# Kernel optimization log

Measured on AMD Instinct MI355X. Metric: run time of the kernel, lower is better.

The kernel has to match this reference:

```python
import jax, jax.numpy as jnp
import numpy as np

N_NODES = 100000
N_EDGES = 1600000
D = 128          # gnn_input_size == gnn_hidden_size
N_LAYERS = 7
N_GRAPHS = 64
N_CLASSES = 10
SNN_IN, SNN_H = 512, 1024
SNN_BETA = 0.85


def setup_inputs() -> dict:
    key = jax.random.key(0)
    ks = jax.random.split(key, 16)
    s = 0.05  # keep activations tame through 7 relu layers
    return {
        "snn_x": jax.random.normal(ks[0], (N_GRAPHS, SNN_IN), jnp.float32),
        "x": jax.random.normal(ks[1], (N_NODES, D), jnp.float32),
        "edge_index": jax.random.randint(ks[2], (2, N_EDGES), 0, N_NODES, jnp.int64),
        "batch": jnp.sort(jax.random.randint(ks[3], (N_NODES,), 0, N_GRAPHS, jnp.int64)),
        "snn_w1": jax.random.normal(ks[4], (SNN_IN, SNN_H), jnp.float32) * s,
        "snn_b1": jax.random.normal(ks[5], (SNN_H,), jnp.float32) * s,
        "snn_w2": jax.random.normal(ks[6], (SNN_H, N_CLASSES), jnp.float32) * s,
        "snn_b2": jax.random.normal(ks[7], (N_CLASSES,), jnp.float32) * s,
        "conv_wrel": jax.random.normal(ks[8], (N_LAYERS, D, D), jnp.float32) * s,
        "conv_wroot": jax.random.normal(ks[9], (N_LAYERS, D, D), jnp.float32) * s,
        "conv_brel": jax.random.normal(ks[10], (N_LAYERS, D), jnp.float32) * s,
        "lin_w": jax.random.normal(ks[11], (D, N_CLASSES), jnp.float32) * s,
        "lin_b": jax.random.normal(ks[12], (N_CLASSES,), jnp.float32) * s,
        "fuse_w": jax.random.normal(ks[13], (2 * N_CLASSES, N_CLASSES), jnp.float32) * s,
        "fuse_b": jax.random.normal(ks[14], (N_CLASSES,), jnp.float32) * s,
    }


def reference(snn_x, x, edge_index, batch,
              snn_w1, snn_b1, snn_w2, snn_b2,
              conv_wrel, conv_wroot, conv_brel,
              lin_w, lin_b, fuse_w, fuse_b):
    n = x.shape[0]
    src, dst = edge_index[0], edge_index[1]
    h = x
    for i in range(conv_wrel.shape[0]):
        agg = jax.ops.segment_sum(h[src], dst, num_segments=n)  # gather + scatter-add
        h = jax.nn.relu(agg @ conv_wrel[i] + conv_brel[i] + h @ conv_wroot[i])
    # global_mean_pool over batch segments
    sums = jax.ops.segment_sum(h, batch, num_segments=N_GRAPHS)
    cnts = jax.ops.segment_sum(jnp.ones((n,), h.dtype), batch, num_segments=N_GRAPHS)
    pooled = sums / jnp.maximum(cnts, 1.0)[:, None]
    gnn_logits = pooled @ lin_w + lin_b
    # SNN branch
    snn_h = jax.nn.relu(snn_x @ snn_w1 + snn_b1)
    snn_logits = SNN_BETA * (snn_h @ snn_w2 + snn_b2)
    # fusion
    fused = jnp.concatenate([snn_logits, gnn_logits], axis=-1)
    return fused @ fuse_w + fuse_b
```

## Files before the change

### kernel.cpp

```cpp
#include <hip/hip_runtime.h>
#include <hip/hip_bf16.h>

#define N_NODES 100000
#define N_EDGES 1600000
#define DIM     128
#define N_LAYERS 7
#define N_GRAPHS 64
#define SNN_IN  512
#define SNN_HID 1024
#define NCLS    10
#define M_PAD   100096
#define MBLK    782
#define NBK     782
#define SORT_CHUNK 4096
#define SORT_NCH   391
#define XPAIRS  (N_NODES * 64)
#define HPAIRS  (M_PAD * 64)
#define WELEMS  (N_LAYERS * DIM * 256)
#define AGG_BLOCKS 2048
#define AGG_WAVES  (AGG_BLOCKS * 4)
#define NQUAD   (N_NODES / 4)
#define POOL2_NB 1564
#define SNN_BLKS 256
#define SS_PAD  2000384

#define AS1 __attribute__((address_space(1)))
#define AS3 __attribute__((address_space(3)))

typedef __attribute__((ext_vector_type(8))) short short8;
typedef __attribute__((ext_vector_type(4))) float f32x4;

__device__ __forceinline__ unsigned int f2bf(float f) {
    unsigned int u = __float_as_uint(f);
    return (u + 0x7fffu + ((u >> 16) & 1u)) >> 16;
}
__device__ __forceinline__ float bf2f(unsigned short b) {
    return __uint_as_float(((unsigned int)b) << 16);
}
__device__ __forceinline__ void acc_pair(unsigned int u, float& lo, float& hi) {
    lo += __uint_as_float(u << 16);
    hi += __uint_as_float(u & 0xffff0000u);
}

__global__ void k_convert(const float* __restrict__ x, const float* __restrict__ wrel,
                          const float* __restrict__ wroot, unsigned int* __restrict__ h,
                          unsigned short* __restrict__ Wt,
                          float* __restrict__ pooled, int* __restrict__ counts) {
    int i = blockIdx.x * blockDim.x + threadIdx.x;
    if (i < N_GRAPHS * 128) pooled[i] = 0.f;
    if (i >= N_GRAPHS * 128 && i < N_GRAPHS * 129) counts[i - N_GRAPHS * 128] = 0;
    if (i < XPAIRS) {
        float2 v = ((const float2*)x)[i];
        h[i] = f2bf(v.x) | (f2bf(v.y) << 16);
    } else if (i < HPAIRS) {
        h[i] = 0u;
    } else {
        int idx = i - HPAIRS;
        if (idx < WELEMS) {
            int l = idx >> 15, rem = idx & 32767, n = rem >> 8, k = rem & 255;
            float v = (k < 128) ? wrel[l * 16384 + k * 128 + n]
                                : wroot[l * 16384 + (k - 128) * 128 + n];
            Wt[idx] = (unsigned short)f2bf(v);
        }
    }
}

__global__ __launch_bounds__(256) void k_histA(const int* __restrict__ dst,
                                               int* __restrict__ chunk_hist) {
    __shared__ int hist[NBK];
    int b = blockIdx.x, t = threadIdx.x;
    int e0 = b * SORT_CHUNK;
    int e1 = e0 + SORT_CHUNK; if (e1 > N_EDGES) e1 = N_EDGES;
    for (int i = t; i < NBK; i += 256) hist[i] = 0;
    __syncthreads();
    for (int e = e0 + t; e < e1; e += 256) atomicAdd(&hist[dst[e] >> 7], 1);
    __syncthreads();
    for (int i = t; i < NBK; i += 256) chunk_hist[b * NBK + i] = hist[i];
}

__global__ __launch_bounds__(64) void k_colscan(int* __restrict__ chunk_hist,
                                                int* __restrict__ btot) {
    int b = blockIdx.x;
    int lane = threadIdx.x;
    const int C = (SORT_NCH + 63) / 64;
    int vals[C]; int sum = 0;
    #pragma unroll
    for (int j = 0; j < C; j++) {
        int c = lane * C + j;
        vals[j] = (c < SORT_NCH) ? chunk_hist[c * NBK + b] : 0;
        sum += vals[j];
    }
    int s = sum;
    #pragma unroll
    for (int o = 1; o < 64; o <<= 1) { int t = __shfl_up(s, o); if (lane >= o) s += t; }
    if (lane == 63) btot[b] = s;
    int run = s - sum;
    #pragma unroll
    for (int j = 0; j < C; j++) {
        int c = lane * C + j;
        if (c < SORT_NCH) chunk_hist[c * NBK + b] = run;
        run += vals[j];
    }
}

__global__ __launch_bounds__(256) void k_bscan(const int* __restrict__ btot,
                                               int* __restrict__ bucket_base) {
    __shared__ int wsum[4];
    int tid = threadIdx.x, lane = tid & 63, wid = tid >> 6;
    int i0 = tid * 4;
    int v[4]; int sum = 0;
    #pragma unroll
    for (int j = 0; j < 4; j++) { int i = i0 + j; v[j] = (i < NBK) ? btot[i] : 0; sum += v[j]; }
    int s = sum;
    #pragma unroll
    for (int o = 1; o < 64; o <<= 1) { int t = __shfl_up(s, o); if (lane >= o) s += t; }
    if (lane == 63) wsum[wid] = s;
    __syncthreads();
    if (tid == 0) {
        int acc = 0;
        #pragma unroll
        for (int w = 0; w < 4; w++) { acc += wsum[w]; wsum[w] = acc; }
    }
    __syncthreads();
    int prefix = s - sum + (wid ? wsum[wid - 1] : 0);
    #pragma unroll
    for (int j = 0; j < 4; j++) { int i = i0 + j; if (i < NBK) bucket_base[i] = prefix; prefix += v[j]; }
}

__global__ __launch_bounds__(256) void k_scatterA(const int* __restrict__ src,
                                                  const int* __restrict__ dst,
                                                  const int* __restrict__ chunk_hist,
                                                  const int* __restrict__ bucket_base,
                                                  unsigned int* __restrict__ pairs) {
    __shared__ int lcur[NBK];
    int b = blockIdx.x, t = threadIdx.x;
    int e0 = b * SORT_CHUNK;
    int e1 = e0 + SORT_CHUNK; if (e1 > N_EDGES) e1 = N_EDGES;
    for (int i = t; i < NBK; i += 256) lcur[i] = chunk_hist[b * NBK + i] + bucket_base[i];
    __syncthreads();
    for (int e = e0 + t; e < e1; e += 256) {
        int d = dst[e];
        int bk = d >> 7;
        int pos = atomicAdd(&lcur[bk], 1);
        pairs[pos] = (unsigned int)src[e] | ((unsigned int)(d & 127) << 17);
    }
}

__global__ __launch_bounds__(256) void k_bucketB(const unsigned int* __restrict__ pairs,
                                                 const int* __restrict__ bucket_base,
                                                 const int* __restrict__ btot,
                                                 int* __restrict__ row_off,
                                                 int* __restrict__ ndeg,
                                                 int* __restrict__ sorted_src) {
    __shared__ int lcnt[128];
    __shared__ int loff[128];
    int b = blockIdx.x, t = threadIdx.x;
    int node0 = b << 7;
    int nn = N_NODES - node0; if (nn > 128) nn = 128;
    int base = bucket_base[b];
    int end  = base + btot[b];
    int pbase = ((base + 3) & ~3) + 512 * b;
    if (t < 128) lcnt[t] = 0;
    __syncthreads();
    for (int i = base + t; i < end; i += 256) atomicAdd(&lcnt[pairs[i] >> 17], 1);
    __syncthreads();
    if (t < 64) {
        int v0 = (lcnt[2 * t] + 3) & ~3, v1 = (lcnt[2 * t + 1] + 3) & ~3;
        int s = v0 + v1, ps = s;
        #pragma unroll
        for (int o = 1; o < 64; o <<= 1) { int u = __shfl_up(ps, o); if (t >= o) ps += u; }
        int excl = ps - s;
        loff[2 * t] = excl; loff[2 * t + 1] = excl + v0;
    }
    __syncthreads();
    if (t < nn) {
        int d = lcnt[t];
        row_off[node0 + t] = pbase + loff[t];
        ndeg[node0 + t] = d;
        int pad = (d + 3) & ~3;
        for (int k = d; k < pad; k++) sorted_src[pbase + loff[t] + k] = N_NODES;
    }
    __syncthreads();
    if (t < 128) lcnt[t] = 0;
    __syncthreads();
    for (int i = base + t; i < end; i += 256) {
        unsigned int p = pairs[i];
        int l = p >> 17;
        int pos = atomicAdd(&lcnt[l], 1);
        sorted_src[pbase + loff[l] + pos] = (int)(p & 0x1FFFFu);
    }
}

#define GATH(d0, d1, d2, d3, s) \
    d0 = *(const uint4*)(hbl + (size_t)(((unsigned)(s).x) << 8)); \
    d1 = *(const uint4*)(hbl + (size_t)(((unsigned)(s).y) << 8)); \
    d2 = *(const uint4*)(hbl + (size_t)(((unsigned)(s).z) << 8)); \
    d3 = *(const uint4*)(hbl + (size_t)(((unsigned)(s).w) << 8));
#define ACC4(r0, r1, r2, r3) \
    acc_pair((r0).x, a[0], a[1]); acc_pair((r0).y, a[2], a[3]); \
    acc_pair((r0).z, a[4], a[5]); acc_pair((r0).w, a[6], a[7]); \
    acc_pair((r1).x, a[0], a[1]); acc_pair((r1).y, a[2], a[3]); \
    acc_pair((r1).z, a[4], a[5]); acc_pair((r1).w, a[6], a[7]); \
    acc_pair((r2).x, a[0], a[1]); acc_pair((r2).y, a[2], a[3]); \
    acc_pair((r2).z, a[4], a[5]); acc_pair((r2).w, a[6], a[7]); \
    acc_pair((r3).x, a[0], a[1]); acc_pair((r3).y, a[2], a[3]); \
    acc_pair((r3).z, a[4], a[5]); acc_pair((r3).w, a[6], a[7]);

__global__ __launch_bounds__(256) void k_agg(const char* __restrict__ hb,
                                             const int* __restrict__ row_off,
                                             const int* __restrict__ ndeg,
                                             const int4* __restrict__ sorted4,
                                             uint4* __restrict__ agg4) {
    int gw = blockIdx.x * 4 + (threadIdx.x >> 6);
    int lane = threadIdx.x & 63;
    int sub = lane >> 4, li = lane & 15;
    const char* hbl = hb + li * 16;
    for (int quad = gw; quad < NQUAD; quad += AGG_WAVES) {
        int node = quad * 4 + sub;
        int beg = row_off[node] >> 2;
        int nit = (ndeg[node] + 3) >> 2;
        float a[8] = {0.f, 0.f, 0.f, 0.f, 0.f, 0.f, 0.f, 0.f};
        if (nit > 0) {
            int4 sa = sorted4[beg];
            int4 sb = sorted4[beg + 1];
            uint4 A0, A1, A2, A3, B0, B1, B2, B3;
            GATH(A0, A1, A2, A3, sa);
            int it = 0;
            for (; it + 2 < nit; it += 2) {
                GATH(B0, B1, B2, B3, sb);
                sa = sorted4[beg + it + 2];
                ACC4(A0, A1, A2, A3);
                GATH(A0, A1, A2, A3, sa);
                sb = sorted4[beg + it + 3];
                ACC4(B0, B1, B2, B3);
            }
            if (it + 1 < nit) {
                GATH(B0, B1, B2, B3, sb);
                ACC4(A0, A1, A2, A3);
                ACC4(B0, B1, B2, B3);
            } else {
                ACC4(A0, A1, A2, A3);
            }
        }
        uint4 o;
        o.x = f2bf(a[0]) | (f2bf(a[1]) << 16);
        o.y = f2bf(a[2]) | (f2bf(a[3]) << 16);
        o.z = f2bf(a[4]) | (f2bf(a[5]) << 16);
        o.w = f2bf(a[6]) | (f2bf(a[7]) << 16);
        agg4[(size_t)node * 16 + li] = o;
    }
}

__global__ __launch_bounds__(256) void k_gemm(const unsigned short* __restrict__ Ag,
                                              const unsigned short* __restrict__ H,
                                              const unsigned short* __restrict__ Wt,
                                              const float* __restrict__ bias,
                                              unsigned short* __restrict__ Hout) {
    __shared__ char smem[65536];
    int tid = threadIdx.x;
    int lane = tid & 63, wid = tid >> 6;
    int wr = (wid >> 1) * 64, wc = (wid & 1) * 64;
    int row0 = blockIdx.x * 128;
    int l4 = lane & 15, hq = lane >> 4;
    f32x4 acc[4][4] = {};

    char* wbase = smem + wid * 16384;
    const unsigned short* bb = Wt + (size_t)(wc + l4) * 256 + hq * 8;

    auto stage = [&](int buf, int kt) {
        const unsigned short* P = (kt < 2) ? Ag : H;
        int kbase = (kt & 1) * 64;
        #pragma unroll
        for (int j = 0; j < 8; j++) {
            int rowl = 8 * j + (lane >> 3);
            int cc = (lane & 7) ^ (rowl & 7);
            const unsigned short* g = P + (size_t)(row0 + wr + rowl) * 128 + kbase + cc * 8;
            char* l = wbase + buf * 8192 + j * 1024;
            __builtin_amdgcn_global_load_lds((const AS1 unsigned int*)g,
                                             (AS3 unsigned int*)l, 16, 0, 0);
        }
    };

    auto compute = [&](int buf, int kt) {
        const char* base = wbase + buf * 8192;
        #pragma unroll
        for (int s2 = 0; s2 < 2; s2++) {
            int sg = kt * 2 + s2;
            short8 a[4], b[4];
            #pragma unroll
            for (int mi = 0; mi < 4; mi++) {
                int rowl = l4 + 16 * mi;
                int ch = (s2 * 4 + hq) ^ (rowl & 7);
                a[mi] = *(const short8*)(base + rowl * 128 + ch * 16);
            }
            #pragma unroll
            for (int ni = 0; ni < 4; ni++)
                b[ni] = *(const short8*)(bb + (size_t)ni * 16 * 256 + sg * 32);
            #pragma unroll
            for (int mi = 0; mi < 4; mi++)
                #pragma unroll
                for (int ni = 0; ni < 4; ni++)
                    acc[mi][ni] = __builtin_amdgcn_mfma_f32_16x16x32_bf16(a[mi], b[ni], acc[mi][ni], 0, 0, 0);
        }
    };

    stage(0, 0);
    #pragma unroll
    for (int kt = 0; kt < 4; kt++) {
        if (kt + 1 < 4) stage((kt + 1) & 1, kt + 1);
        __builtin_amdgcn_sched_barrier(0);
        if (kt < 3) asm volatile("s_waitcnt vmcnt(8)" ::: "memory");
        else        asm volatile("s_waitcnt vmcnt(0)" ::: "memory");
        __builtin_amdgcn_sched_barrier(0);
        compute(kt & 1, kt);
    }

    unsigned short* Es = (unsigned short*)smem;
    int cb = wc + l4;
    int rs = hq * 4;
    #pragma unroll
    for (int p = 0; p < 2; ++p) {
        __syncthreads();
        if (wr == 64 * p) {
            #pragma unroll
            for (int ni = 0; ni < 4; ni++) {
                int col = cb + ni * 16;
                float bn = bias[col];
                #pragma unroll
                for (int mi = 0; mi < 4; mi++) {
                    int rloc = mi * 16 + rs;
                    #pragma unroll
                    for (int rr = 0; rr < 4; rr++) {
                        float v = acc[mi][ni][rr] + bn;
                        v = v > 0.f ? v : 0.f;
                        if (row0 + 64 * p + rloc + rr >= N_NODES) v = 0.f;
                        Es[(rloc + rr) * 144 + col] = (unsigned short)f2bf(v);
                    }
                }
            }
        }
        __syncthreads();
        int rloc = tid >> 2;
        int c4 = (tid & 3) * 4;
        uint4* gd = (uint4*)(Hout + (size_t)(row0 + 64 * p + rloc) * 128);
        const uint4* es = (const uint4*)(Es + (size_t)rloc * 144);
        #pragma unroll
        for (int j = 0; j < 4; j++) gd[c4 + j] = es[c4 + j];
    }
}

__global__ __launch_bounds__(256) void k_pool_snn(const unsigned short* __restrict__ h,
                                                  const int* __restrict__ batch,
                                                  float* __restrict__ pooled,
                                                  int* __restrict__ counts,
                                                  const float* __restrict__ x,
                                                  const float* __restrict__ w1,
                                                  const float* __restrict__ b1,
                                                  float* __restrict__ snn_out) {
    if (blockIdx.x < POOL2_NB) {
        int start = blockIdx.x * 64;
        if (start >= N_NODES) return;
        __shared__ int bsh[64];
        int t = threadIdx.x;
        int end = start + 64; if (end > N_NODES) end = N_NODES;
        int nn = end - start;
        if (t < nn) bsh[t] = batch[start + t];
        __syncthreads();
        int dim = t & 127, seg = t >> 7;
        int i0 = seg * 32, i1 = i0 + 32; if (i1 > nn) i1 = nn;
        float acc = 0.f; int cur = -1, cnt = 0;
        for (int i = i0; i < i1; i++) {
            int g = bsh[i];
            if (g != cur) {
                if (cur >= 0) {
                    atomicAdd(&pooled[cur * 128 + dim], acc);
                    if (dim == 0) atomicAdd(&counts[cur], cnt);
                }
                cur = g; acc = 0.f; cnt = 0;
            }
            acc += bf2f(h[(size_t)(start + i) * 128 + dim]);
            cnt++;
        }
        if (cur >= 0) {
            atomicAdd(&pooled[cur * 128 + dim], acc);
            if (dim == 0) atomicAdd(&counts[cur], cnt);
        }
    } else {
        int m2 = blockIdx.x - POOL2_NB;
        int m = m2 >> 2, cc = m2 & 3;
        __shared__ float xs[SNN_IN];
        int tid = threadIdx.x;
        for (int i = tid; i < SNN_IN; i += 256) xs[i] = x[m * SNN_IN + i];
        __syncthreads();
        int c = cc * 256 + tid;
        float a = 0.f;
        for (int k = 0; k < SNN_IN; k++) a += xs[k] * w1[(size_t)k * SNN_HID + c];
        float v = a + b1[c];
        snn_out[m * SNN_HID + c] = v > 0.f ? v : 0.f;
    }
}

__global__ __launch_bounds__(64) void k_head(const float* __restrict__ pooled, const int* __restrict__ counts,
                                             const float* __restrict__ lin_w, const float* __restrict__ lin_b,
                                             const float* __restrict__ snn_h, const float* __restrict__ w2,
                                             const float* __restrict__ b2, const float* __restrict__ fuse_w,
                                             const float* __restrict__ fuse_b, float* __restrict__ out) {
    int m = blockIdx.x, lane = threadIdx.x;
    __shared__ float sm[20];
    float cnt = (float)(counts[m] > 0 ? counts[m] : 1);
    float p0 = pooled[m * 128 + lane] / cnt;
    float p1 = pooled[m * 128 + 64 + lane] / cnt;
    for (int c = 0; c < NCLS; c++) {
        float v = p0 * lin_w[lane * 10 + c] + p1 * lin_w[(lane + 64) * 10 + c];
        #pragma unroll
        for (int o = 32; o > 0; o >>= 1) v += __shfl_down(v, o);
        if (lane == 0) sm[10 + c] = v + lin_b[c];
    }
    for (int c = 0; c < NCLS; c++) {
        float v = 0.f;
        #pragma unroll
        for (int j = 0; j < 16; j++) {
            int k = lane + j * 64;
            v += snn_h[m * SNN_HID + k] * w2[k * 10 + c];
        }
        #pragma unroll
        for (int o = 32; o > 0; o >>= 1) v += __shfl_down(v, o);
        if (lane == 0) sm[c] = 0.85f * (v + b2[c]);
    }
    __syncthreads();
    if (lane < NCLS) {
        float o = fuse_b[lane];
        #pragma unroll
        for (int j = 0; j < 20; j++) o += sm[j] * fuse_w[j * 10 + lane];
        out[m * 10 + lane] = o;
    }
}

extern "C" void kernel_launch(void* const* d_in, const int* in_sizes, int n_in,
                              void* d_out, int out_size, void* d_ws, size_t ws_size,
                              hipStream_t stream) {
    const float* snn_x  = (const float*)d_in[0];
    const float* x      = (const float*)d_in[1];
    const int*   ei     = (const int*)d_in[2];
    const int*   batch  = (const int*)d_in[3];
    const float* w1     = (const float*)d_in[4];
    const float* b1     = (const float*)d_in[5];
    const float* w2     = (const float*)d_in[6];
    const float* b2     = (const float*)d_in[7];
    const float* wrel   = (const float*)d_in[8];
    const float* wroot  = (const float*)d_in[9];
    const float* brel   = (const float*)d_in[10];
    const float* lin_w  = (const float*)d_in[11];
    const float* lin_b  = (const float*)d_in[12];
    const float* fuse_w = (const float*)d_in[13];
    const float* fuse_b = (const float*)d_in[14];
    const int* srcv = ei;
    const int* dstv = ei + N_EDGES;

    char* ws = (char*)d_ws;
    size_t off = 0;
    auto alloc = [&](size_t b) { char* p = ws + off; off = (off + b + 255) & ~(size_t)255; return p; };
    unsigned short* h0   = (unsigned short*)alloc((size_t)M_PAD * 128 * 2);
    unsigned short* h1   = (unsigned short*)alloc((size_t)M_PAD * 128 * 2);
    unsigned short* agg  = (unsigned short*)alloc((size_t)M_PAD * 128 * 2);
    unsigned short* Wt   = (unsigned short*)alloc((size_t)N_LAYERS * 128 * 256 * 2);
    int* sorted_src = (int*)alloc((size_t)SS_PAD * 4 + 16);
    unsigned int* pairs = (unsigned int*)alloc((size_t)N_EDGES * 4);
    int* chunk_hist = (int*)alloc((size_t)SORT_NCH * NBK * 4);
    int* row_off    = (int*)alloc((size_t)(N_NODES + 1) * 4);
    int* ndeg       = (int*)alloc((size_t)N_NODES * 4);
    int* btot       = (int*)alloc((size_t)NBK * 4);
    int* bucket_base= (int*)alloc((size_t)NBK * 4);
    float* pooled   = (float*)alloc((size_t)N_GRAPHS * 128 * 4);
    int* counts     = (int*)alloc((size_t)N_GRAPHS * 4);
    float* snn_h    = (float*)alloc((size_t)N_GRAPHS * SNN_HID * 4);

    k_histA<<<SORT_NCH, 256, 0, stream>>>(dstv, chunk_hist);
    k_colscan<<<NBK, 64, 0, stream>>>(chunk_hist, btot);
    k_bscan<<<1, 256, 0, stream>>>(btot, bucket_base);
    k_scatterA<<<SORT_NCH, 256, 0, stream>>>(srcv, dstv, chunk_hist, bucket_base, pairs);
    k_bucketB<<<NBK, 256, 0, stream>>>(pairs, bucket_base, btot, row_off, ndeg, sorted_src);
    k_convert<<<(HPAIRS + WELEMS + 255) / 256, 256, 0, stream>>>(x, wrel, wroot, (unsigned int*)h0,
                                                                 Wt, pooled, counts);

    unsigned short* hc = h0;
    unsigned short* hn = h1;
    for (int l = 0; l < N_LAYERS; l++) {
        k_agg<<<AGG_BLOCKS, 256, 0, stream>>>((const char*)hc, row_off, ndeg,
                                              (const int4*)sorted_src, (uint4*)agg);
        k_gemm<<<MBLK, 256, 0, stream>>>(agg, hc, Wt + (size_t)l * 128 * 256, brel + l * 128, hn);
        unsigned short* t = hc; hc = hn; hn = t;
    }
    k_pool_snn<<<POOL2_NB + SNN_BLKS, 256, 0, stream>>>(hc, batch, pooled, counts,
                                                        snn_x, w1, b1, snn_h);
    k_head<<<N_GRAPHS, 64, 0, stream>>>(pooled, counts, lin_w, lin_b, snn_h, w2, b2, fuse_w, fuse_b,
                                        (float*)d_out);
}
```

Measured before the change: 842.8 us.

## Stage full A tile cooperatively in LDS and drop per-wave double buffering

The GEMM kernel used to have each wave stream its own 64-row A slice through a double-buffered LDS region, overlapping loads with MFMA work. It now has all four waves load the whole 128x256 concatenated [agg|h] tile into LDS in one pass, then synchronise and run all eight k-steps from LDS. Waves that share rows no longer load them separately, which cuts duplicate global traffic, and the vmcnt pipelining logic goes away. The cost is losing the overlap between loads and compute, plus a block-wide barrier before any math starts.

```diff
diff --git a/kernel.cpp b/kernel.cpp
--- a/kernel.cpp
+++ b/kernel.cpp
@@ -264,55 +264,44 @@
     int l4 = lane & 15, hq = lane >> 4;
     f32x4 acc[4][4] = {};
 
-    char* wbase = smem + wid * 16384;
     const unsigned short* bb = Wt + (size_t)(wc + l4) * 256 + hq * 8;
 
-    auto stage = [&](int buf, int kt) {
-        const unsigned short* P = (kt < 2) ? Ag : H;
-        int kbase = (kt & 1) * 64;
-        #pragma unroll
-        for (int j = 0; j < 8; j++) {
-            int rowl = 8 * j + (lane >> 3);
-            int cc = (lane & 7) ^ (rowl & 7);
-            const unsigned short* g = P + (size_t)(row0 + wr + rowl) * 128 + kbase + cc * 8;
-            char* l = wbase + buf * 8192 + j * 1024;
+    {
+        int r_off = lane >> 5;
+        int half = (lane >> 4) & 1;
+        const unsigned short* P = half ? H : Ag;
+        #pragma unroll
+        for (int i = 0; i < 16; i++) {
+            int r0 = wid * 32 + i * 2;
+            int r = r0 + r_off;
+            int c = (lane & 15) ^ (r & 7);
+            const char* g = (const char*)(P + (size_t)(row0 + r) * 128) + c * 16;
+            char* ldst = smem + r0 * 512;
             __builtin_amdgcn_global_load_lds((const AS1 unsigned int*)g,
-                                             (AS3 unsigned int*)l, 16, 0, 0);
-        }
-    };
-
-    auto compute = [&](int buf, int kt) {
-        const char* base = wbase + buf * 8192;
-        #pragma unroll
-        for (int s2 = 0; s2 < 2; s2++) {
-            int sg = kt * 2 + s2;
-            short8 a[4], b[4];
-            #pragma unroll
-            for (int mi = 0; mi < 4; mi++) {
-                int rowl = l4 + 16 * mi;
-                int ch = (s2 * 4 + hq) ^ (rowl & 7);
-                a[mi] = *(const short8*)(base + rowl * 128 + ch * 16);
-            }
+                                             (AS3 unsigned int*)ldst, 16, 0, 0);
+        }
+    }
+    __syncthreads();
+
+    #pragma unroll
+    for (int sg = 0; sg < 8; sg++) {
+        short8 a[4], b[4];
+        int halfoff = (sg < 4) ? 0 : 256;
+        int cbase = (sg & 3) * 4 + hq;
+        #pragma unroll
+        for (int mi = 0; mi < 4; mi++) {
+            int row = wr + l4 + 16 * mi;
+            int p = cbase ^ (row & 7);
+            a[mi] = *(const short8*)(smem + (size_t)row * 512 + halfoff + p * 16);
+        }
+        #pragma unroll
+        for (int ni = 0; ni < 4; ni++)
+            b[ni] = *(const short8*)(bb + (size_t)ni * 16 * 256 + sg * 32);
+        #pragma unroll
+        for (int mi = 0; mi < 4; mi++)
             #pragma unroll
             for (int ni = 0; ni < 4; ni++)
-                b[ni] = *(const short8*)(bb + (size_t)ni * 16 * 256 + sg * 32);
-            #pragma unroll
-            for (int mi = 0; mi < 4; mi++)
-                #pragma unroll
-                for (int ni = 0; ni < 4; ni++)
-                    acc[mi][ni] = __builtin_amdgcn_mfma_f32_16x16x32_bf16(a[mi], b[ni], acc[mi][ni], 0, 0, 0);
-        }
-    };
-
-    stage(0, 0);
-    #pragma unroll
-    for (int kt = 0; kt < 4; kt++) {
-        if (kt + 1 < 4) stage((kt + 1) & 1, kt + 1);
-        __builtin_amdgcn_sched_barrier(0);
-        if (kt < 3) asm volatile("s_waitcnt vmcnt(8)" ::: "memory");
-        else        asm volatile("s_waitcnt vmcnt(0)" ::: "memory");
-        __builtin_amdgcn_sched_barrier(0);
-        compute(kt & 1, kt);
+                acc[mi][ni] = __builtin_amdgcn_mfma_f32_16x16x32_bf16(a[mi], b[ni], acc[mi][ni], 0, 0, 0);
     }
 
     unsigned short* Es = (unsigned short*)smem;
```

New measurement: 864.6 us. +2.6%, slower.
